# Kernel optimization log

Measured on AMD Instinct MI355X. Metric: run time of the kernel, lower is better.

The kernel has to match this reference:

```python
import jax, jax.numpy as jnp
import numpy as np

N_NODES = 20000
N_EDGES = 50000
NF = 64
NG = 5
N_CONV = 2


def setup_inputs() -> dict:
    key = jax.random.key(0)
    ks = jax.random.split(key, 20)
    s = 0.1
    return {
        "h": jax.random.normal(ks[0], (N_NODES, 64), jnp.float32),
        "edge_index": jax.random.randint(ks[1], (2, N_EDGES), 0, N_NODES, jnp.int64),
        "edge_weight": jax.random.uniform(ks[2], (N_EDGES,), jnp.float32),
        "edge_attr": jax.random.normal(ks[3], (N_EDGES, NG), jnp.float32),
        # lin0: Linear(64 -> nf); stored as [in, out]
        "lin0_w": jax.random.normal(ks[4], (64, NF), jnp.float32) * s,
        "lin0_b": jnp.zeros((NF,), jnp.float32),
        # short: Linear(num_gaussians -> nf)
        "short_w": jax.random.normal(ks[5], (NG, NF), jnp.float32) * s,
        "short_b": jnp.zeros((NF,), jnp.float32),
        # edge network nn: Linear(nf -> nf//4) -> ReLU -> Linear(nf//4 -> nf*nf)
        "nn1_w": jax.random.normal(ks[6], (NF, NF // 4), jnp.float32) * s,
        "nn1_b": jnp.zeros((NF // 4,), jnp.float32),
        "nn2_w": jax.random.normal(ks[7], (NF // 4, NF * NF), jnp.float32) * s,
        "nn2_b": jnp.zeros((NF * NF,), jnp.float32),
        # NNConv root weight (Linear(nf, nf, bias=False)) + conv bias
        "root_w": jax.random.normal(ks[8], (NF, NF), jnp.float32) * s,
        "conv_bias": jnp.zeros((NF,), jnp.float32),
        # GRU(nf, nf): torch packs gates as [r; z; n] along dim 0 of [3*nf, nf]
        "gru_w_ih": jax.random.normal(ks[9], (NF, 3 * NF), jnp.float32) * s,
        "gru_w_hh": jax.random.normal(ks[10], (NF, 3 * NF), jnp.float32) * s,
        "gru_b_ih": jnp.zeros((3 * NF,), jnp.float32),
        "gru_b_hh": jnp.zeros((3 * NF,), jnp.float32),
    }


def _gru_cell(x, h, w_ih, w_hh, b_ih, b_hh):
    gi = x @ w_ih + b_ih            # [N, 3*nf]
    gh = h @ w_hh + b_hh
    r = jax.nn.sigmoid(gi[:, :NF] + gh[:, :NF])
    z = jax.nn.sigmoid(gi[:, NF:2 * NF] + gh[:, NF:2 * NF])
    n = jnp.tanh(gi[:, 2 * NF:] + r * gh[:, 2 * NF:])
    return (1.0 - z) * n + z * h


def reference(h, edge_index, edge_weight, edge_attr,
              lin0_w, lin0_b, short_w, short_b,
              nn1_w, nn1_b, nn2_w, nn2_b,
              root_w, conv_bias,
              gru_w_ih, gru_w_hh, gru_b_ih, gru_b_hh):
    n_nodes = h.shape[0]
    src, dst = edge_index[0], edge_index[1]

    out = jax.nn.relu(h @ lin0_w + lin0_b)                       # [N, nf]
    ea = jax.nn.relu(edge_attr @ short_w + short_b)              # [E, nf]

    # edge-conditioned weights (fixed per forward since edge_attr is fixed)
    w_e = (jax.nn.relu(ea @ nn1_w + nn1_b) @ nn2_w + nn2_b)      # [E, nf*nf]
    w_e = w_e.reshape(-1, NF, NF)                                # [E, nf, nf]

    # scatter-mean denominator (clamped to 1 like PyG)
    cnt = jax.ops.segment_sum(jnp.ones_like(dst, jnp.float32), dst,
                              num_segments=n_nodes)
    cnt = jnp.maximum(cnt, 1.0)[:, None]                          # [N, 1]

    hidden = out                                                  # GRU state [N, nf]
    for _ in range(N_CONV):
        x_j = out[src]                                            # gather [E, nf]
        msg = jnp.einsum('ef,efg->eg', x_j, w_e)                  # per-edge matmul
        agg = jax.ops.segment_sum(msg, dst, num_segments=n_nodes) / cnt
        conv = agg + out @ root_w + conv_bias                     # root + bias
        m = jax.nn.relu(conv)
        hidden = _gru_cell(m, hidden, gru_w_ih, gru_w_hh, gru_b_ih, gru_b_hh)
        out = hidden
    return out
```

## Files before the change

kernel.cpp:

```cpp
#include <hip/hip_runtime.h>

#define N_NODES 20000
#define N_EDGES 50000
#define NPB 16
#define KCAP 16
#define NTILE (N_NODES / NPB)

#define ZB 79
#define PB 416
#define LB 625
#define ETB 1563
#define VB0 (ZB + PB + LB + ETB)
#define HB 196

typedef __attribute__((ext_vector_type(8))) short short8;
typedef __attribute__((ext_vector_type(4))) float f32x4;
typedef unsigned int u32;
typedef unsigned short u16;

#define SswzB(i, o) (((i) * 2304 + (o)) ^ (((i) & 7) << 4))
#define MofsB(i, o) ((20480 + (i) * 256 + (o)) ^ (((i) & 7) << 4))

struct Pars {
    const float* h; const int* ei; const float* eattr;
    const float *lin0w, *lin0b, *shw, *shb, *w1, *b1, *w2, *b2;
    const float *rootw, *convb, *wih, *whh, *bih, *bhh;
    u16 *X0b, *X1b;
    float* out;
    u16 *t_arr, *Bp1, *Bp2;
    int* cur; u32* edata;
};

__device__ inline u16 f2bf(float x) {
    u32 u = __float_as_uint(x);
    return (u16)((u + 0x7FFFu + ((u >> 16) & 1u)) >> 16);
}
__device__ inline float bf2f(u16 v) { return __uint_as_float((u32)v << 16); }

__device__ inline void acc_edge(float* acc, const u16* t, float x) {
    uint4 a = *(const uint4*)t, b = *(const uint4*)(t + 8);
    u32 tw[8] = {a.x, a.y, a.z, a.w, b.x, b.y, b.z, b.w};
#pragma unroll
    for (int q = 0; q < 8; ++q) {
        acc[2 * q]     += __uint_as_float(tw[q] << 16) * x;
        acc[2 * q + 1] += __uint_as_float(tw[q] & 0xFFFF0000u) * x;
    }
}

__global__ __launch_bounds__(256) void k_stageA(Pars p) {
    __shared__ float sh[32][64];
    int tid = threadIdx.x;
    int vb = blockIdx.x;
    if (vb < ZB) {
        int n = vb * 256 + tid;
        if (n < N_NODES) p.cur[n] = 0;
        return;
    }
    vb -= ZB;
    if (vb < PB) {
        int idx = vb * 256 + tid;
        if (idx < 73728) {
            int j = idx & 7, l = (idx >> 3) & 63, rest = idx >> 9;
            int kb = rest % 36, nt = rest / 36;
            int row = kb * 32 + (l >> 4) * 8 + j;
            int col = nt * 16 + (l & 15);
            float v;
            if (row < 1024) v = p.w2[row * 64 + col];
            else if (row < 1088) v = p.b2[(row - 1024) * 64 + col];
            else v = p.rootw[(row - 1088) * 64 + col];
            p.Bp1[idx] = f2bf(v);
        } else {
            int o = idx - 73728;
            int j = o & 7, l = (o >> 3) & 63, rest = o >> 9;
            int kb = rest & 3, nt = rest >> 2;
            int k2 = kb * 32 + (l >> 4) * 8 + j;
            int c = nt * 16 + (l & 15);
            float v;
            if (k2 < 64) {
                v = (c < 192) ? p.wih[k2 * 192 + c] : 0.f;
            } else {
                int f = k2 - 64;
                v = (c < 128) ? p.whh[f * 192 + c] : ((c < 192) ? 0.f : p.whh[f * 192 + c - 64]);
            }
            p.Bp2[o] = f2bf(v);
        }
        return;
    }
    vb -= PB;
    int g = tid & 63, q = tid >> 6;
    if (vb < LB) {
        int n0 = vb * 32;
        for (int i = tid; i < 32 * 64; i += 256) sh[i >> 6][i & 63] = p.h[n0 * 64 + i];
        __syncthreads();
        float bias = p.lin0b[g];
        float acc[8];
#pragma unroll
        for (int j = 0; j < 8; j++) acc[j] = bias;
        for (int f = 0; f < 64; f++) {
            float wv = p.lin0w[f * 64 + g];
#pragma unroll
            for (int j = 0; j < 8; j++) acc[j] += sh[q * 8 + j][f] * wv;
        }
#pragma unroll
        for (int j = 0; j < 8; j++) {
            float a = acc[j];
            p.X0b[(n0 + q * 8 + j) * 64 + g] = f2bf(a > 0.f ? a : 0.f);
        }
        return;
    }
    vb -= LB;
    {
        int e0 = vb * 32;
#pragma unroll
        for (int j = 0; j < 8; j++) {
            int r = q * 8 + j;
            int e = e0 + r;
            if (e < N_EDGES) {
                float a0 = p.eattr[e * 5 + 0], a1 = p.eattr[e * 5 + 1], a2 = p.eattr[e * 5 + 2],
                      a3 = p.eattr[e * 5 + 3], a4 = p.eattr[e * 5 + 4];
                float v = p.shb[g] + a0 * p.shw[g] + a1 * p.shw[64 + g] + a2 * p.shw[128 + g]
                        + a3 * p.shw[192 + g] + a4 * p.shw[256 + g];
                sh[r][g] = v > 0.f ? v : 0.f;
            }
        }
        __syncthreads();
#pragma unroll
        for (int jj = 0; jj < 2; jj++) {
            int r = q * 8 + (g >> 4) * 2 + jj;
            int e = e0 + r;
            int o = g & 15;
            if (e < N_EDGES) {
                float acc = p.b1[o];
                for (int c = 0; c < 64; c++) acc += sh[r][c] * p.w1[c * 16 + o];
                float t = acc > 0.f ? acc : 0.f;
                p.t_arr[(size_t)e * 16 + o] = f2bf(t);
            }
        }
    }
}

__global__ __launch_bounds__(256) void k_stageB(Pars p) {
    int e = blockIdx.x * 256 + threadIdx.x;
    if (e < N_EDGES) {
        int dn = p.ei[N_EDGES + e];
        int q = atomicAdd(&p.cur[dn], 1);
        if (q < KCAP) p.edata[dn * KCAP + q] = ((u32)e << 15) | (u32)p.ei[e];
    }
}

__global__ __launch_bounds__(256, 4) void k_convK(Pars p, const u16* __restrict__ Xprev,
                                                  u16* __restrict__ XoutB,
                                                  float* __restrict__ XoutF) {
    __shared__ __align__(16) char smem[36864];
    float* G = (float*)smem;
    char* Sb = smem;
    int tid = threadIdx.x, g = tid & 63, wq = tid >> 6;
    int m16 = g & 15, hi4 = g >> 4;
    int n0 = blockIdx.x * NPB;

    int cvv[4];
    u16 xrb[4];
    float ic4[4];
#pragma unroll
    for (int jj = 0; jj < 4; ++jj) {
        int n = n0 + wq * 4 + jj;
        int c = __builtin_amdgcn_readfirstlane(p.cur[n]);
        cvv[jj] = c < KCAP ? c : KCAP;
        ic4[jj] = 1.0f / (c > 0 ? (float)c : 1.0f);
        xrb[jj] = Xprev[n * 64 + g];
    }

    short8 a2x[2];
#pragma unroll
    for (int kb = 0; kb < 2; ++kb)
        a2x[kb] = *(const short8*)(Xprev + (size_t)(n0 + m16) * 64 + kb * 32 + hi4 * 8);

    for (int jj = 0; jj < 4; ++jj) {
        int i = wq * 4 + jj;
        float acc[16];
#pragma unroll
        for (int k = 0; k < 16; ++k) acc[k] = 0.f;
        float sx = 0.f;
        int base = (n0 + i) * KCAP;
        int cv = cvv[jj];
        for (int pp = 0; pp < cv; pp += 4) {
            int m = cv - pp;
            uint4 ed = *(const uint4*)(p.edata + base + pp);
            u32 k0 = ed.x;
            u32 k1 = m > 1 ? ed.y : ed.x;
            u32 k2 = m > 2 ? ed.z : ed.x;
            u32 k3 = m > 3 ? ed.w : ed.x;
            float x0 = bf2f(Xprev[(k0 & 0x7FFFu) * 64 + g]);
            float x1 = m > 1 ? bf2f(Xprev[(k1 & 0x7FFFu) * 64 + g]) : 0.f;
            float x2 = m > 2 ? bf2f(Xprev[(k2 & 0x7FFFu) * 64 + g]) : 0.f;
            float x3 = m > 3 ? bf2f(Xprev[(k3 & 0x7FFFu) * 64 + g]) : 0.f;
            acc_edge(acc, p.t_arr + (size_t)(k0 >> 15) * 16, x0);
            acc_edge(acc, p.t_arr + (size_t)(k1 >> 15) * 16, x1);
            acc_edge(acc, p.t_arr + (size_t)(k2 >> 15) * 16, x2);
            acc_edge(acc, p.t_arr + (size_t)(k3 >> 15) * 16, x3);
            sx += x0 + x1 + x2 + x3;
        }
        float ic = ic4[jj];
#pragma unroll
        for (int k = 0; k < 16; ++k)
            *(u16*)(Sb + SswzB(i, k * 128 + g * 2)) = f2bf(acc[k] * ic);
        *(u16*)(Sb + SswzB(i, 2048 + g * 2)) = f2bf(sx * ic);
        *(u16*)(Sb + SswzB(i, 2176 + g * 2)) = xrb[jj];
    }
    __syncthreads();

    f32x4 d = {0.f, 0.f, 0.f, 0.f};
#pragma unroll
    for (int kb = 0; kb < 36; ++kb) {
        short8 a = *(const short8*)(Sb + SswzB(m16, kb * 64 + hi4 * 16));
        short8 b = *(const short8*)((const char*)p.Bp1 + ((size_t)(wq * 36 + kb) * 64 + g) * 16);
        d = __builtin_amdgcn_mfma_f32_16x16x32_bf16(a, b, d, 0, 0, 0);
    }
    __syncthreads();

    {
        float cb = p.convb[wq * 16 + m16];
#pragma unroll
        for (int r = 0; r < 4; ++r) {
            float m = d[r] + cb;
            m = m > 0.f ? m : 0.f;
            *(u16*)(smem + MofsB(hi4 * 4 + r, (wq * 16 + m16) * 2)) = f2bf(m);
        }
    }
    __syncthreads();

    short8 a2[4];
#pragma unroll
    for (int kb = 0; kb < 2; ++kb)
        a2[kb] = *(const short8*)(smem + MofsB(m16, kb * 64 + hi4 * 16));
    a2[2] = a2x[0];
    a2[3] = a2x[1];
    f32x4 e4[4];
#pragma unroll
    for (int q = 0; q < 4; ++q) { e4[q].x = 0.f; e4[q].y = 0.f; e4[q].z = 0.f; e4[q].w = 0.f; }
#pragma unroll
    for (int q = 0; q < 4; ++q)
#pragma unroll
        for (int kb = 0; kb < 4; ++kb) {
            short8 b = *(const short8*)((const char*)p.Bp2 + ((size_t)((wq * 4 + q) * 4 + kb) * 64 + g) * 16);
            e4[q] = __builtin_amdgcn_mfma_f32_16x16x32_bf16(a2[kb], b, e4[q], 0, 0, 0);
        }
#pragma unroll
    for (int q = 0; q < 4; ++q)
#pragma unroll
        for (int r = 0; r < 4; ++r)
            G[(hi4 * 4 + r) * 260 + wq * 64 + q * 16 + m16] = e4[q][r];
    __syncthreads();

    float b_r = p.bih[g] + p.bhh[g];
    float b_z = p.bih[64 + g] + p.bhh[64 + g];
    float b_gi = p.bih[128 + g];
    float b_gh = p.bhh[128 + g];
#pragma unroll
    for (int jj = 0; jj < 4; ++jj) {
        int i = wq * 4 + jj;
        int n = n0 + i;
        float rs = G[i * 260 + g] + b_r;
        float zs = G[i * 260 + 64 + g] + b_z;
        float gi = G[i * 260 + 128 + g] + b_gi;
        float gh = G[i * 260 + 192 + g] + b_gh;
        float r = 1.f / (1.f + __expf(-rs));
        float z = 1.f / (1.f + __expf(-zs));
        float aa = gi + r * gh;
        float ex = __expf(2.f * aa);
        float nt = 1.f - 2.f / (ex + 1.f);
        float res = (1.f - z) * nt + z * bf2f(xrb[jj]);
        if (XoutF) XoutF[n * 64 + g] = res;
        else       XoutB[n * 64 + g] = f2bf(res);
    }
}

extern "C" void kernel_launch(void* const* d_in, const int* in_sizes, int n_in,
                              void* d_out, int out_size, void* d_ws, size_t ws_size,
                              hipStream_t stream) {
    Pars p;
    p.h     = (const float*)d_in[0];
    p.ei    = (const int*)d_in[1];
    p.eattr = (const float*)d_in[3];
    p.lin0w = (const float*)d_in[4];
    p.lin0b = (const float*)d_in[5];
    p.shw   = (const float*)d_in[6];
    p.shb   = (const float*)d_in[7];
    p.w1    = (const float*)d_in[8];
    p.b1    = (const float*)d_in[9];
    p.w2    = (const float*)d_in[10];
    p.b2    = (const float*)d_in[11];
    p.rootw = (const float*)d_in[12];
    p.convb = (const float*)d_in[13];
    p.wih   = (const float*)d_in[14];
    p.whh   = (const float*)d_in[15];
    p.bih   = (const float*)d_in[16];
    p.bhh   = (const float*)d_in[17];

    char* ws = (char*)d_ws;
    p.X0b   = (u16*)ws;   ws += (size_t)N_NODES * 64 * 2;
    p.X1b   = (u16*)ws;   ws += (size_t)N_NODES * 64 * 2;
    p.t_arr = (u16*)ws;   ws += (size_t)N_EDGES * 16 * 2;
    p.Bp1   = (u16*)ws;   ws += (size_t)73728 * 2;
    p.Bp2   = (u16*)ws;   ws += (size_t)32768 * 2;
    p.cur   = (int*)ws;   ws += (size_t)N_NODES * 4;
    p.edata = (u32*)ws;   ws += (size_t)N_NODES * KCAP * 4;
    p.out   = (float*)d_out;

    k_stageA<<<VB0, 256, 0, stream>>>(p);
    k_stageB<<<HB, 256, 0, stream>>>(p);
    k_convK<<<NTILE, 256, 0, stream>>>(p, p.X0b, p.X1b, nullptr);
    k_convK<<<NTILE, 256, 0, stream>>>(p, p.X1b, nullptr, p.out);
}
```

Before: 87.34 us.

## Double conv block to 512 threads with split-K MFMA and LDS reduction

Each conv block now launches 8 waves instead of 4, so every wave gathers neighbour messages for 2 nodes instead of 4. Both MFMA GEMMs split their K dimension across two wave halves, and the partial results are reduced through shared memory before the bias/ReLU and GRU steps. The goal is more latency hiding in the gather-heavy aggregation and shorter per-wave serial work. In exchange it adds an extra LDS round trip, more barriers, and reworked shared-memory offsets to fit the partial buffers.

```diff
diff --git a/kernel.cpp b/kernel.cpp
--- a/kernel.cpp
+++ b/kernel.cpp
@@ -19,7 +19,7 @@
 typedef unsigned short u16;
 
 #define SswzB(i, o) (((i) * 2304 + (o)) ^ (((i) & 7) << 4))
-#define MofsB(i, o) ((20480 + (i) * 256 + (o)) ^ (((i) & 7) << 4))
+#define MofsB(i, o) ((32768 + (i) * 256 + (o)) ^ (((i) & 7) << 4))
 
 struct Pars {
     const float* h; const int* ei; const float* eattr;
@@ -148,35 +148,33 @@
     }
 }
 
-__global__ __launch_bounds__(256, 4) void k_convK(Pars p, const u16* __restrict__ Xprev,
+__global__ __launch_bounds__(512, 8) void k_convK(Pars p, const u16* __restrict__ Xprev,
                                                   u16* __restrict__ XoutB,
                                                   float* __restrict__ XoutF) {
     __shared__ __align__(16) char smem[36864];
+    char* Sb = smem;
+    float* DP = (float*)smem;
     float* G = (float*)smem;
-    char* Sb = smem;
     int tid = threadIdx.x, g = tid & 63, wq = tid >> 6;
+    int gate = wq & 3, khalf = wq >> 2;
     int m16 = g & 15, hi4 = g >> 4;
     int n0 = blockIdx.x * NPB;
 
-    int cvv[4];
-    u16 xrb[4];
-    float ic4[4];
-#pragma unroll
-    for (int jj = 0; jj < 4; ++jj) {
-        int n = n0 + wq * 4 + jj;
+    int cvv[2];
+    u16 xrb[2];
+    float ic2[2];
+#pragma unroll
+    for (int jj = 0; jj < 2; ++jj) {
+        int n = n0 + wq * 2 + jj;
         int c = __builtin_amdgcn_readfirstlane(p.cur[n]);
         cvv[jj] = c < KCAP ? c : KCAP;
-        ic4[jj] = 1.0f / (c > 0 ? (float)c : 1.0f);
+        ic2[jj] = 1.0f / (c > 0 ? (float)c : 1.0f);
         xrb[jj] = Xprev[n * 64 + g];
     }
 
-    short8 a2x[2];
-#pragma unroll
-    for (int kb = 0; kb < 2; ++kb)
-        a2x[kb] = *(const short8*)(Xprev + (size_t)(n0 + m16) * 64 + kb * 32 + hi4 * 8);
-
-    for (int jj = 0; jj < 4; ++jj) {
-        int i = wq * 4 + jj;
+#pragma unroll
+    for (int jj = 0; jj < 2; ++jj) {
+        int i = wq * 2 + jj;
         float acc[16];
 #pragma unroll
         for (int k = 0; k < 16; ++k) acc[k] = 0.f;
@@ -200,7 +198,7 @@
             acc_edge(acc, p.t_arr + (size_t)(k3 >> 15) * 16, x3);
             sx += x0 + x1 + x2 + x3;
         }
-        float ic = ic4[jj];
+        float ic = ic2[jj];
 #pragma unroll
         for (int k = 0; k < 16; ++k)
             *(u16*)(Sb + SswzB(i, k * 128 + g * 2)) = f2bf(acc[k] * ic);
@@ -211,45 +209,54 @@
 
     f32x4 d = {0.f, 0.f, 0.f, 0.f};
 #pragma unroll
-    for (int kb = 0; kb < 36; ++kb) {
+    for (int kk = 0; kk < 18; ++kk) {
+        int kb = khalf * 18 + kk;
         short8 a = *(const short8*)(Sb + SswzB(m16, kb * 64 + hi4 * 16));
-        short8 b = *(const short8*)((const char*)p.Bp1 + ((size_t)(wq * 36 + kb) * 64 + g) * 16);
+        short8 b = *(const short8*)((const char*)p.Bp1 + ((size_t)(gate * 36 + kb) * 64 + g) * 16);
         d = __builtin_amdgcn_mfma_f32_16x16x32_bf16(a, b, d, 0, 0, 0);
     }
     __syncthreads();
-
-    {
-        float cb = p.convb[wq * 16 + m16];
-#pragma unroll
-        for (int r = 0; r < 4; ++r) {
-            float m = d[r] + cb;
-            m = m > 0.f ? m : 0.f;
-            *(u16*)(smem + MofsB(hi4 * 4 + r, (wq * 16 + m16) * 2)) = f2bf(m);
-        }
-    }
-    __syncthreads();
-
-    short8 a2[4];
-#pragma unroll
-    for (int kb = 0; kb < 2; ++kb)
-        a2[kb] = *(const short8*)(smem + MofsB(m16, kb * 64 + hi4 * 16));
-    a2[2] = a2x[0];
-    a2[3] = a2x[1];
+#pragma unroll
+    for (int r = 0; r < 4; ++r)
+        DP[khalf * 1024 + (hi4 * 4 + r) * 64 + gate * 16 + m16] = d[r];
+    __syncthreads();
+
+#pragma unroll
+    for (int t2 = 0; t2 < 2; ++t2) {
+        int idx = tid + t2 * 512;
+        int i = idx >> 6, c = idx & 63;
+        float m = DP[i * 64 + c] + DP[1024 + i * 64 + c] + p.convb[c];
+        m = m > 0.f ? m : 0.f;
+        *(u16*)(smem + MofsB(i, c * 2)) = f2bf(m);
+    }
+    __syncthreads();
+
+    short8 a2[2];
+    if (khalf == 0) {
+#pragma unroll
+        for (int t = 0; t < 2; ++t)
+            a2[t] = *(const short8*)(smem + MofsB(m16, t * 64 + hi4 * 16));
+    } else {
+#pragma unroll
+        for (int t = 0; t < 2; ++t)
+            a2[t] = *(const short8*)(Xprev + (size_t)(n0 + m16) * 64 + t * 32 + hi4 * 8);
+    }
     f32x4 e4[4];
 #pragma unroll
     for (int q = 0; q < 4; ++q) { e4[q].x = 0.f; e4[q].y = 0.f; e4[q].z = 0.f; e4[q].w = 0.f; }
 #pragma unroll
     for (int q = 0; q < 4; ++q)
 #pragma unroll
-        for (int kb = 0; kb < 4; ++kb) {
-            short8 b = *(const short8*)((const char*)p.Bp2 + ((size_t)((wq * 4 + q) * 4 + kb) * 64 + g) * 16);
-            e4[q] = __builtin_amdgcn_mfma_f32_16x16x32_bf16(a2[kb], b, e4[q], 0, 0, 0);
+        for (int t = 0; t < 2; ++t) {
+            int kb2 = khalf * 2 + t;
+            short8 b = *(const short8*)((const char*)p.Bp2 + ((size_t)((gate * 4 + q) * 4 + kb2) * 64 + g) * 16);
+            e4[q] = __builtin_amdgcn_mfma_f32_16x16x32_bf16(a2[t], b, e4[q], 0, 0, 0);
         }
 #pragma unroll
     for (int q = 0; q < 4; ++q)
 #pragma unroll
         for (int r = 0; r < 4; ++r)
-            G[(hi4 * 4 + r) * 260 + wq * 64 + q * 16 + m16] = e4[q][r];
+            G[khalf * 4096 + (hi4 * 4 + r) * 256 + gate * 64 + q * 16 + m16] = e4[q][r];
     __syncthreads();
 
     float b_r = p.bih[g] + p.bhh[g];
@@ -257,13 +264,13 @@
     float b_gi = p.bih[128 + g];
     float b_gh = p.bhh[128 + g];
 #pragma unroll
-    for (int jj = 0; jj < 4; ++jj) {
-        int i = wq * 4 + jj;
+    for (int jj = 0; jj < 2; ++jj) {
+        int i = wq * 2 + jj;
         int n = n0 + i;
-        float rs = G[i * 260 + g] + b_r;
-        float zs = G[i * 260 + 64 + g] + b_z;
-        float gi = G[i * 260 + 128 + g] + b_gi;
-        float gh = G[i * 260 + 192 + g] + b_gh;
+        float rs = G[i * 256 + g]        + G[4096 + i * 256 + g]        + b_r;
+        float zs = G[i * 256 + 64 + g]   + G[4096 + i * 256 + 64 + g]   + b_z;
+        float gi = G[i * 256 + 128 + g]  + G[4096 + i * 256 + 128 + g]  + b_gi;
+        float gh = G[i * 256 + 192 + g]  + G[4096 + i * 256 + 192 + g]  + b_gh;
         float r = 1.f / (1.f + __expf(-rs));
         float z = 1.f / (1.f + __expf(-zs));
         float aa = gi + r * gh;
@@ -309,6 +316,6 @@
 
     k_stageA<<<VB0, 256, 0, stream>>>(p);
     k_stageB<<<HB, 256, 0, stream>>>(p);
-    k_convK<<<NTILE, 256, 0, stream>>>(p, p.X0b, p.X1b, nullptr);
-    k_convK<<<NTILE, 256, 0, stream>>>(p, p.X1b, nullptr, p.out);
-}
+    k_convK<<<NTILE, 512, 0, stream>>>(p, p.X0b, p.X1b, nullptr);
+    k_convK<<<NTILE, 512, 0, stream>>>(p, p.X1b, nullptr, p.out);
+}
```

Measured after the change: 93.74 us. +7.3%, slower.

## Process 32 nodes per block with 512 threads, reusing B fragments across two M tiles

Applied to the files above, without the earlier changes.

Doubles the node tile from 16 to 32 per block and launches 512 threads. Only the first four waves run the MFMA stages, each computing two 16-row tiles so every loaded B fragment from Bp1/Bp2 feeds two MFMAs, halving weight traffic per node. The cost is half the waves idling during the matmul phases, LDS use per block doubling to 72KB which limits occupancy, and half as many blocks in the grid.

```diff
diff --git a/kernel.cpp b/kernel.cpp
--- a/kernel.cpp
+++ b/kernel.cpp
@@ -2,7 +2,7 @@
 
 #define N_NODES 20000
 #define N_EDGES 50000
-#define NPB 16
+#define NPB 32
 #define KCAP 16
 #define NTILE (N_NODES / NPB)
 
@@ -19,7 +19,7 @@
 typedef unsigned short u16;
 
 #define SswzB(i, o) (((i) * 2304 + (o)) ^ (((i) & 7) << 4))
-#define MofsB(i, o) ((20480 + (i) * 256 + (o)) ^ (((i) & 7) << 4))
+#define MofsB(i, o) ((36864 + (i) * 256 + (o)) ^ (((i) & 7) << 4))
 
 struct Pars {
     const float* h; const int* ei; const float* eattr;
@@ -148,12 +148,12 @@
     }
 }
 
-__global__ __launch_bounds__(256, 4) void k_convK(Pars p, const u16* __restrict__ Xprev,
+__global__ __launch_bounds__(512, 4) void k_convK(Pars p, const u16* __restrict__ Xprev,
                                                   u16* __restrict__ XoutB,
                                                   float* __restrict__ XoutF) {
-    __shared__ __align__(16) char smem[36864];
+    __shared__ __align__(16) char smem[73728];
+    char* Sb = smem;
     float* G = (float*)smem;
-    char* Sb = smem;
     int tid = threadIdx.x, g = tid & 63, wq = tid >> 6;
     int m16 = g & 15, hi4 = g >> 4;
     int n0 = blockIdx.x * NPB;
@@ -170,11 +170,7 @@
         xrb[jj] = Xprev[n * 64 + g];
     }
 
-    short8 a2x[2];
-#pragma unroll
-    for (int kb = 0; kb < 2; ++kb)
-        a2x[kb] = *(const short8*)(Xprev + (size_t)(n0 + m16) * 64 + kb * 32 + hi4 * 8);
-
+#pragma unroll
     for (int jj = 0; jj < 4; ++jj) {
         int i = wq * 4 + jj;
         float acc[16];
@@ -209,47 +205,65 @@
     }
     __syncthreads();
 
-    f32x4 d = {0.f, 0.f, 0.f, 0.f};
-#pragma unroll
-    for (int kb = 0; kb < 36; ++kb) {
-        short8 a = *(const short8*)(Sb + SswzB(m16, kb * 64 + hi4 * 16));
-        short8 b = *(const short8*)((const char*)p.Bp1 + ((size_t)(wq * 36 + kb) * 64 + g) * 16);
-        d = __builtin_amdgcn_mfma_f32_16x16x32_bf16(a, b, d, 0, 0, 0);
+    f32x4 d0 = {0.f, 0.f, 0.f, 0.f}, d1 = {0.f, 0.f, 0.f, 0.f};
+    if (wq < 4) {
+#pragma unroll
+        for (int kb = 0; kb < 36; ++kb) {
+            short8 b = *(const short8*)((const char*)p.Bp1 + ((size_t)(wq * 36 + kb) * 64 + g) * 16);
+            short8 a0 = *(const short8*)(Sb + SswzB(m16, kb * 64 + hi4 * 16));
+            short8 a1 = *(const short8*)(Sb + SswzB(16 + m16, kb * 64 + hi4 * 16));
+            d0 = __builtin_amdgcn_mfma_f32_16x16x32_bf16(a0, b, d0, 0, 0, 0);
+            d1 = __builtin_amdgcn_mfma_f32_16x16x32_bf16(a1, b, d1, 0, 0, 0);
+        }
     }
     __syncthreads();
 
-    {
+    if (wq < 4) {
         float cb = p.convb[wq * 16 + m16];
 #pragma unroll
         for (int r = 0; r < 4; ++r) {
-            float m = d[r] + cb;
-            m = m > 0.f ? m : 0.f;
-            *(u16*)(smem + MofsB(hi4 * 4 + r, (wq * 16 + m16) * 2)) = f2bf(m);
+            float m0 = d0[r] + cb;
+            m0 = m0 > 0.f ? m0 : 0.f;
+            *(u16*)(smem + MofsB(hi4 * 4 + r, (wq * 16 + m16) * 2)) = f2bf(m0);
+            float m1 = d1[r] + cb;
+            m1 = m1 > 0.f ? m1 : 0.f;
+            *(u16*)(smem + MofsB(16 + hi4 * 4 + r, (wq * 16 + m16) * 2)) = f2bf(m1);
         }
     }
     __syncthreads();
 
-    short8 a2[4];
-#pragma unroll
-    for (int kb = 0; kb < 2; ++kb)
-        a2[kb] = *(const short8*)(smem + MofsB(m16, kb * 64 + hi4 * 16));
-    a2[2] = a2x[0];
-    a2[3] = a2x[1];
-    f32x4 e4[4];
-#pragma unroll
-    for (int q = 0; q < 4; ++q) { e4[q].x = 0.f; e4[q].y = 0.f; e4[q].z = 0.f; e4[q].w = 0.f; }
-#pragma unroll
-    for (int q = 0; q < 4; ++q)
-#pragma unroll
-        for (int kb = 0; kb < 4; ++kb) {
-            short8 b = *(const short8*)((const char*)p.Bp2 + ((size_t)((wq * 4 + q) * 4 + kb) * 64 + g) * 16);
-            e4[q] = __builtin_amdgcn_mfma_f32_16x16x32_bf16(a2[kb], b, e4[q], 0, 0, 0);
-        }
-#pragma unroll
-    for (int q = 0; q < 4; ++q)
-#pragma unroll
-        for (int r = 0; r < 4; ++r)
-            G[(hi4 * 4 + r) * 260 + wq * 64 + q * 16 + m16] = e4[q][r];
+    if (wq < 4) {
+        short8 a2[2][4];
+#pragma unroll
+        for (int mt = 0; mt < 2; ++mt) {
+#pragma unroll
+            for (int t = 0; t < 2; ++t)
+                a2[mt][t] = *(const short8*)(smem + MofsB(mt * 16 + m16, t * 64 + hi4 * 16));
+#pragma unroll
+            for (int t = 0; t < 2; ++t)
+                a2[mt][2 + t] = *(const short8*)(Xprev + (size_t)(n0 + mt * 16 + m16) * 64 + t * 32 + hi4 * 8);
+        }
+        f32x4 e4[2][4];
+#pragma unroll
+        for (int mt = 0; mt < 2; ++mt)
+#pragma unroll
+            for (int q = 0; q < 4; ++q) { e4[mt][q].x = 0.f; e4[mt][q].y = 0.f; e4[mt][q].z = 0.f; e4[mt][q].w = 0.f; }
+#pragma unroll
+        for (int q = 0; q < 4; ++q)
+#pragma unroll
+            for (int kb = 0; kb < 4; ++kb) {
+                short8 b = *(const short8*)((const char*)p.Bp2 + ((size_t)((wq * 4 + q) * 4 + kb) * 64 + g) * 16);
+                e4[0][q] = __builtin_amdgcn_mfma_f32_16x16x32_bf16(a2[0][kb], b, e4[0][q], 0, 0, 0);
+                e4[1][q] = __builtin_amdgcn_mfma_f32_16x16x32_bf16(a2[1][kb], b, e4[1][q], 0, 0, 0);
+            }
+#pragma unroll
+        for (int mt = 0; mt < 2; ++mt)
+#pragma unroll
+            for (int q = 0; q < 4; ++q)
+#pragma unroll
+                for (int r = 0; r < 4; ++r)
+                    G[mt * 4160 + (hi4 * 4 + r) * 260 + wq * 64 + q * 16 + m16] = e4[mt][q][r];
+    }
     __syncthreads();
 
     float b_r = p.bih[g] + p.bhh[g];
@@ -260,10 +274,11 @@
     for (int jj = 0; jj < 4; ++jj) {
         int i = wq * 4 + jj;
         int n = n0 + i;
-        float rs = G[i * 260 + g] + b_r;
-        float zs = G[i * 260 + 64 + g] + b_z;
-        float gi = G[i * 260 + 128 + g] + b_gi;
-        float gh = G[i * 260 + 192 + g] + b_gh;
+        const float* Gi = G + (i >> 4) * 4160 + (i & 15) * 260;
+        float rs = Gi[g] + b_r;
+        float zs = Gi[64 + g] + b_z;
+        float gi = Gi[128 + g] + b_gi;
+        float gh = Gi[192 + g] + b_gh;
         float r = 1.f / (1.f + __expf(-rs));
         float z = 1.f / (1.f + __expf(-zs));
         float aa = gi + r * gh;
@@ -309,6 +324,6 @@
 
     k_stageA<<<VB0, 256, 0, stream>>>(p);
     k_stageB<<<HB, 256, 0, stream>>>(p);
-    k_convK<<<NTILE, 256, 0, stream>>>(p, p.X0b, p.X1b, nullptr);
-    k_convK<<<NTILE, 256, 0, stream>>>(p, p.X1b, nullptr, p.out);
-}
+    k_convK<<<NTILE, 512, 0, stream>>>(p, p.X0b, p.X1b, nullptr);
+    k_convK<<<NTILE, 512, 0, stream>>>(p, p.X1b, nullptr, p.out);
+}
```

Result: slower. 91.43 us (+4.7%).
